# Performance work log

Hardware: AMD Instinct MI355X
Metric: run time of the kernel (lower is better)

The kernel has to match this reference:

```python
import jax, jax.numpy as jnp
import numpy as np

K, N, D, NCONV, E = 3, 30000, 128, 6, 480000


def _graph_conv(x, src, dst, ew, Wp, bp, Wrel, Wroot):
    # SAGE-style project=True: pre-project+relu source features
    h = jax.nn.relu(x @ Wp + bp)                    # [N, D]
    msg = ew[:, None] * h[src]                      # [E, D] gather
    agg = jax.ops.segment_sum(msg, dst, num_segments=N)
    cnt = jax.ops.segment_sum(jnp.ones_like(ew), dst, num_segments=N)
    agg = agg / jnp.maximum(cnt, 1.0)[:, None]      # mean aggregation
    return agg @ Wrel + x @ Wroot                   # GraphConv: lin_rel(agg)+lin_root(x), bias=False


def setup_inputs() -> dict:
    key = jax.random.key(0)
    ks = jax.random.split(key, 16)
    w = lambda k, s: (jax.random.normal(k, s, jnp.float32) * 0.05)
    inp = {
        "H_K_prev": jax.random.normal(ks[0], (K, N, D), jnp.float32),
        "edgelists": jax.random.randint(ks[1], (K, 2, E), 0, N, jnp.int32),
        "spec_weight": jax.random.uniform(ks[2], (K, NCONV, E), jnp.float32),
        # 6 stacked GraphConv params
        "Wp": w(ks[3], (NCONV, D, D)),
        "bp": jnp.zeros((NCONV, D), jnp.float32),
        "Wrel": w(ks[4], (NCONV, D, D)),
        "Wroot": w(ks[5], (NCONV, D, D)),
        # combine projection (7D -> 3D) and proj_linear (4D -> D)
        "W_comb": w(ks[6], ((NCONV + 1) * D, 3 * D)),
        "b_comb": jnp.zeros((3 * D,), jnp.float32),
        "W_pl": w(ks[7], (4 * D, D)),
        "b_pl": jnp.zeros((D,), jnp.float32),
        # LSTM (torch gate order i,f,g,o)
        "Wih": w(ks[8], (4 * D, D)),
        "Whh": w(ks[9], (4 * D, D)),
        "bih": jnp.zeros((4 * D,), jnp.float32),
        "bhh": jnp.zeros((4 * D,), jnp.float32),
    }
    return inp


def reference(H_K_prev, edgelists, spec_weight, Wp, bp, Wrel, Wroot,
              W_comb, b_comb, W_pl, b_pl, Wih, Whh, bih, bhh):
    outs = []
    for k in range(K):  # fixed small history loop
        Hk = H_K_prev[k]
        src, dst = edgelists[k, 0], edgelists[k, 1]
        feats = [Hk] + [
            _graph_conv(Hk, src, dst, spec_weight[k, i],
                        Wp[i], bp[i], Wrel[i], Wroot[i])
            for i in range(NCONV)
        ]
        cat = jnp.concatenate(feats, axis=1)               # [N, 7D]
        proj = jax.nn.relu(cat @ W_comb + b_comb)          # [N, 3D] (dropout=eval identity)
        outs.append(jnp.concatenate([Hk, proj], axis=1) @ W_pl + b_pl)  # [N, D]
    xs = jnp.stack(outs, 0)                                # [K, N, D] time-major

    def cell(carry, x_t):
        h, c = carry
        gates = x_t @ Wih.T + h @ Whh.T + bih + bhh        # [N, 4D]
        i, f, g, o = jnp.split(gates, 4, axis=1)
        c = jax.nn.sigmoid(f) * c + jax.nn.sigmoid(i) * jnp.tanh(g)
        h = jax.nn.sigmoid(o) * jnp.tanh(c)
        return (h, c), None

    z = jnp.zeros((N, D), xs.dtype)
    (h, _), _ = jax.lax.scan(cell, (z, z), xs)
    return jax.nn.relu(h)[None]                            # [1, N, D]
```

## Files before the change

kernel.cpp:

```cpp
#include <hip/hip_runtime.h>
#include <math.h>

constexpr int NN  = 30000;
constexpr int DIM = 128;
constexpr int KH  = 3;
constexpr int NC  = 6;
constexpr int EE  = 480000;
constexpr int NBLK = (NN + 255) / 256;

typedef __attribute__((ext_vector_type(8))) short short8;
typedef __attribute__((ext_vector_type(4))) float f32x4;
typedef __attribute__((ext_vector_type(2))) float f32x2;

__device__ __forceinline__ unsigned short f2bf(float f) {
    union { float f; unsigned int i; } c; c.f = f;
    unsigned int u = c.i;
    return (unsigned short)((u + 0x7fffu + ((u >> 16) & 1u)) >> 16);
}
__device__ __forceinline__ float bf2f(unsigned int u) {
    union { unsigned int i; float f; } c; c.i = u << 16; return c.f;
}
__device__ __forceinline__ unsigned int packbf(float x, float y) {
    return (unsigned int)f2bf(x) | ((unsigned int)f2bf(y) << 16);
}
__device__ __forceinline__ float fsig(float x) {
    return __builtin_amdgcn_rcpf(1.f + __expf(-x));
}
__device__ __forceinline__ float ftanh(float x) {
    return 2.f * fsig(2.f * x) - 1.f;
}

template<int OUT, bool RELU>
__global__ __launch_bounds__(256) void mgemm(
    const unsigned short* __restrict__ A1, int lda1,
    const unsigned short* __restrict__ A2, int lda2, int ksplit,
    const unsigned short* __restrict__ Bt, int ldb,
    const float* __restrict__ bias,
    void* __restrict__ Cv, int ldc,
    int M, int K, int nx)
{
    __shared__ __align__(16) unsigned char smem[2 * 128 * 80];
    unsigned char* As = smem;
    unsigned char* Bs = smem + 128 * 80;

    const int nwg  = gridDim.x;
    const int orig = blockIdx.x;
    const int q = nwg >> 3, r = nwg & 7;
    const int xcd = orig & 7, idx = orig >> 3;
    const int lin = (xcd < r ? xcd * (q + 1) : r * (q + 1) + (xcd - r) * q) + idx;
    const int bx = lin % nx, by = lin / nx;

    const int tid  = threadIdx.x;
    const int lane = tid & 63;
    const int w    = tid >> 6;
    const int wm   = w >> 1, wn = w & 1;
    const int lm   = lane & 15, lg = lane >> 4;
    const int bm   = by * 128;
    const int bn   = bx * 128;

    const int srow  = tid >> 1;
    const int shalf = tid & 1;

    f32x4 acc[4][4] = {};

    int arow = bm + srow; if (arow > M - 1) arow = M - 1;
    const int brow = bn + srow;

    for (int k0 = 0; k0 < K; k0 += 32) {
        const unsigned short* Ap; int la; int kk;
        if (k0 < ksplit) { Ap = A1; la = lda1; kk = k0; }
        else             { Ap = A2; la = lda2; kk = k0 - ksplit; }
        const float4* ga = (const float4*)(Ap + (size_t)arow * la + kk + shalf * 16);
        float4 a0 = ga[0], a1 = ga[1];
        const float4* gb = (const float4*)(Bt + (size_t)brow * ldb + k0 + shalf * 16);
        float4 b0 = gb[0], b1 = gb[1];

        __syncthreads();
        *(float4*)(As + srow * 80 + shalf * 32)      = a0;
        *(float4*)(As + srow * 80 + shalf * 32 + 16) = a1;
        *(float4*)(Bs + srow * 80 + shalf * 32)      = b0;
        *(float4*)(Bs + srow * 80 + shalf * 32 + 16) = b1;
        __syncthreads();

        short8 av[4], bv[4];
        #pragma unroll
        for (int f = 0; f < 4; ++f) {
            av[f] = *(const short8*)(As + (wm * 64 + f * 16 + lm) * 80 + lg * 16);
            bv[f] = *(const short8*)(Bs + (wn * 64 + f * 16 + lm) * 80 + lg * 16);
        }
        #pragma unroll
        for (int i = 0; i < 4; ++i)
            #pragma unroll
            for (int j = 0; j < 4; ++j)
                acc[i][j] = __builtin_amdgcn_mfma_f32_16x16x32_bf16(
                    av[i], bv[j], acc[i][j], 0, 0, 0);
    }

    #pragma unroll
    for (int i = 0; i < 4; ++i) {
        int row0 = bm + wm * 64 + i * 16 + lg * 4;
        #pragma unroll
        for (int j = 0; j < 4; ++j) {
            int col = bn + wn * 64 + j * 16 + lm;
            float bb = bias[col];
            #pragma unroll
            for (int r = 0; r < 4; ++r) {
                int row = row0 + r;
                if (row < M) {
                    float v = acc[i][j][r] + bb;
                    if (RELU) v = fmaxf(v, 0.f);
                    if (OUT == 0) {
                        ((unsigned short*)Cv)[(size_t)row * ldc + col] = f2bf(v);
                    } else {
                        unsigned int pk = __builtin_amdgcn_cvt_pk_fp8_f32(v, v, 0, false);
                        ((unsigned char*)Cv)[(size_t)row * ldc + col] = (unsigned char)pk;
                    }
                }
            }
        }
    }
}

__global__ void hist_kernel(const int* __restrict__ dst, int* __restrict__ cnt, int e)
{
    int i = blockIdx.x * 256 + threadIdx.x;
    if (i < e) atomicAdd(&cnt[dst[i]], 1);
}

__global__ __launch_bounds__(256) void scan_part(const int* __restrict__ cnt,
                                                 int* __restrict__ off,
                                                 int* __restrict__ bsum, int n)
{
    int lane = threadIdx.x & 63, wid = threadIdx.x >> 6;
    int i = blockIdx.x * 256 + threadIdx.x;
    int v = (i < n) ? cnt[i] : 0;
    int x = v;
    #pragma unroll
    for (int ofs = 1; ofs < 64; ofs <<= 1) {
        int t = __shfl_up(x, ofs, 64);
        if (lane >= ofs) x += t;
    }
    __shared__ int ws[4];
    if (lane == 63) ws[wid] = x;
    __syncthreads();
    int wo = 0;
    for (int j = 0; j < wid; ++j) wo += ws[j];
    if (i < n) off[i] = wo + x - v;
    if (threadIdx.x == 255) bsum[blockIdx.x] = wo + x;
}

__global__ __launch_bounds__(128) void scan_tops(const int* __restrict__ bsum,
                                                 int* __restrict__ btop, int nb)
{
    __shared__ int buf[128];
    int v = (threadIdx.x < nb) ? bsum[threadIdx.x] : 0;
    buf[threadIdx.x] = v;
    __syncthreads();
    #pragma unroll
    for (int ofs = 1; ofs < 128; ofs <<= 1) {
        int t = (threadIdx.x >= ofs) ? buf[threadIdx.x - ofs] : 0;
        __syncthreads();
        buf[threadIdx.x] += t;
        __syncthreads();
    }
    if (threadIdx.x < nb) btop[threadIdx.x] = buf[threadIdx.x] - v;
}

__global__ __launch_bounds__(256) void scan_add(int* __restrict__ off,
                                                const int* __restrict__ btop,
                                                int* __restrict__ cursor,
                                                int* __restrict__ cnt, int n)
{
    int i = blockIdx.x * 256 + threadIdx.x;
    if (i < n) {
        int o = off[i] + btop[blockIdx.x];
        off[i] = o;
        cursor[i] = o;
        cnt[i] = 0;
    }
    if (blockIdx.x == 0 && threadIdx.x == 0) off[n] = EE;
}

__global__ void fill_kernel(const int* __restrict__ src, const int* __restrict__ dst,
                            const float* __restrict__ sw,
                            int* __restrict__ cursor, int* __restrict__ csr_src,
                            uint2* __restrict__ swp, int e)
{
    int i = blockIdx.x * 256 + threadIdx.x;
    if (i >= e) return;
    int pos = atomicAdd(&cursor[dst[i]], 1);
    csr_src[pos] = src[i];
    uint2 lo, hi;
    lo.x = packbf(sw[i],                   sw[(size_t)EE + i]);
    lo.y = packbf(sw[2 * (size_t)EE + i],  0.f);
    hi.x = packbf(sw[3 * (size_t)EE + i],  sw[4 * (size_t)EE + i]);
    hi.y = packbf(sw[5 * (size_t)EE + i],  0.f);
    swp[(size_t)pos * 2]     = lo;
    swp[(size_t)pos * 2 + 1] = hi;
}

__global__ __launch_bounds__(256) void gather6(
    const unsigned char* __restrict__ h8,
    const uint2* __restrict__ swp,
    const int* __restrict__ csr_src,
    const int* __restrict__ off,
    unsigned short* __restrict__ agg)
{
    int wid  = threadIdx.x >> 6;
    int lane = threadIdx.x & 63;
    int node = blockIdx.x * 2 + (wid >> 1);
    int half = wid & 1;
    if (node >= NN) return;
    int s0 = off[node], s1 = off[node + 1];
    float a0 = 0.f, a1 = 0.f, b0 = 0.f, b1 = 0.f, c0 = 0.f, c1 = 0.f;
    const size_t hofs = (size_t)half * 384 + (size_t)lane * 2;

    int e = s0;
    for (; e + 3 < s1; e += 4) {
        int sA = csr_src[e],     sB = csr_src[e + 1];
        int sC = csr_src[e + 2], sD = csr_src[e + 3];
        uint2 wA = swp[(size_t)(e    ) * 2 + half];
        uint2 wB = swp[(size_t)(e + 1) * 2 + half];
        uint2 wC = swp[(size_t)(e + 2) * 2 + half];
        uint2 wD = swp[(size_t)(e + 3) * 2 + half];
        const unsigned short* rA = (const unsigned short*)(h8 + (size_t)sA * 768 + hofs);
        const unsigned short* rB = (const unsigned short*)(h8 + (size_t)sB * 768 + hofs);
        const unsigned short* rC = (const unsigned short*)(h8 + (size_t)sC * 768 + hofs);
        const unsigned short* rD = (const unsigned short*)(h8 + (size_t)sD * 768 + hofs);
        unsigned int pA0 = rA[0], pA1 = rA[64], pA2 = rA[128];
        unsigned int pB0 = rB[0], pB1 = rB[64], pB2 = rB[128];
        unsigned int pC0 = rC[0], pC1 = rC[64], pC2 = rC[128];
        unsigned int pD0 = rD[0], pD1 = rD[64], pD2 = rD[128];

        {
            float w0 = bf2f(wA.x & 0xffffu), w1 = bf2f(wA.x >> 16), w2 = bf2f(wA.y & 0xffffu);
            f32x2 h0 = __builtin_amdgcn_cvt_pk_f32_fp8(pA0, false);
            f32x2 h1 = __builtin_amdgcn_cvt_pk_f32_fp8(pA1, false);
            f32x2 h2 = __builtin_amdgcn_cvt_pk_f32_fp8(pA2, false);
            a0 += w0 * h0.x; a1 += w0 * h0.y;
            b0 += w1 * h1.x; b1 += w1 * h1.y;
            c0 += w2 * h2.x; c1 += w2 * h2.y;
        }
        {
            float w0 = bf2f(wB.x & 0xffffu), w1 = bf2f(wB.x >> 16), w2 = bf2f(wB.y & 0xffffu);
            f32x2 h0 = __builtin_amdgcn_cvt_pk_f32_fp8(pB0, false);
            f32x2 h1 = __builtin_amdgcn_cvt_pk_f32_fp8(pB1, false);
            f32x2 h2 = __builtin_amdgcn_cvt_pk_f32_fp8(pB2, false);
            a0 += w0 * h0.x; a1 += w0 * h0.y;
            b0 += w1 * h1.x; b1 += w1 * h1.y;
            c0 += w2 * h2.x; c1 += w2 * h2.y;
        }
        {
            float w0 = bf2f(wC.x & 0xffffu), w1 = bf2f(wC.x >> 16), w2 = bf2f(wC.y & 0xffffu);
            f32x2 h0 = __builtin_amdgcn_cvt_pk_f32_fp8(pC0, false);
            f32x2 h1 = __builtin_amdgcn_cvt_pk_f32_fp8(pC1, false);
            f32x2 h2 = __builtin_amdgcn_cvt_pk_f32_fp8(pC2, false);
            a0 += w0 * h0.x; a1 += w0 * h0.y;
            b0 += w1 * h1.x; b1 += w1 * h1.y;
            c0 += w2 * h2.x; c1 += w2 * h2.y;
        }
        {
            float w0 = bf2f(wD.x & 0xffffu), w1 = bf2f(wD.x >> 16), w2 = bf2f(wD.y & 0xffffu);
            f32x2 h0 = __builtin_amdgcn_cvt_pk_f32_fp8(pD0, false);
            f32x2 h1 = __builtin_amdgcn_cvt_pk_f32_fp8(pD1, false);
            f32x2 h2 = __builtin_amdgcn_cvt_pk_f32_fp8(pD2, false);
            a0 += w0 * h0.x; a1 += w0 * h0.y;
            b0 += w1 * h1.x; b1 += w1 * h1.y;
            c0 += w2 * h2.x; c1 += w2 * h2.y;
        }
    }
    for (; e < s1; ++e) {
        int src = csr_src[e];
        uint2 wv = swp[(size_t)e * 2 + half];
        float w0 = bf2f(wv.x & 0xffffu);
        float w1 = bf2f(wv.x >> 16);
        float w2 = bf2f(wv.y & 0xffffu);
        const unsigned short* hrow = (const unsigned short*)(h8 + (size_t)src * 768 + hofs);
        unsigned int p0 = hrow[0];
        unsigned int p1 = hrow[64];
        unsigned int p2 = hrow[128];
        f32x2 h0 = __builtin_amdgcn_cvt_pk_f32_fp8(p0, false);
        f32x2 h1 = __builtin_amdgcn_cvt_pk_f32_fp8(p1, false);
        f32x2 h2 = __builtin_amdgcn_cvt_pk_f32_fp8(p2, false);
        a0 += w0 * h0.x; a1 += w0 * h0.y;
        b0 += w1 * h1.x; b1 += w1 * h1.y;
        c0 += w2 * h2.x; c1 += w2 * h2.y;
    }
    float inv = 1.f / fmaxf((float)(s1 - s0), 1.f);
    unsigned int* orow = (unsigned int*)(agg + (size_t)node * 768) + 192 * half + lane;
    orow[0]   = packbf(a0 * inv, a1 * inv);
    orow[64]  = packbf(b0 * inv, b1 * inv);
    orow[128] = packbf(c0 * inv, c1 * inv);
}

__global__ void cvt_h(const float* __restrict__ Hk, unsigned int* __restrict__ out,
                      int total)
{
    int idx = blockIdx.x * 256 + threadIdx.x;
    if (idx >= total) return;
    float2 v = ((const float2*)Hk)[idx];
    out[idx] = packbf(v.x, v.y);
}

#define SWA32(r, b) ((r) * 512 + ((b) ^ (((r) & 7) << 4)))

__global__ __launch_bounds__(512) void lstm_fused(
    const unsigned short* __restrict__ xs,
    const unsigned short* __restrict__ Wt,
    const float* __restrict__ bsum,
    float* __restrict__ outp)
{
    __shared__ __align__(16) unsigned char AL[32 * 512];

    const int tid  = threadIdx.x;
    const int lane = tid & 63;
    const int w    = tid >> 6;
    const int lm   = lane & 15, lg = lane >> 4;
    const int node0 = blockIdx.x * 32;

    float bias[4];
    #pragma unroll
    for (int g = 0; g < 4; ++g)
        bias[g] = bsum[w * 64 + g * 16 + lm];

    short8 bw[8][4];
    #pragma unroll
    for (int ks = 0; ks < 8; ++ks)
        #pragma unroll
        for (int g = 0; g < 4; ++g)
            bw[ks][g] = *(const short8*)(Wt +
                (size_t)(w * 64 + g * 16 + lm) * 256 + ks * 32 + lg * 8);

    float cst[2][4] = {};

    float4 z4 = make_float4(0.f, 0.f, 0.f, 0.f);
    {
        int r = tid >> 4, gi = tid & 15;
        *(float4*)(AL + SWA32(r, 256 + gi * 16)) = z4;
    }

    for (int t = 0; t < KH; ++t) {
        const unsigned short* xsrc = xs + (size_t)t * NN * 128;
        {
            int r = tid >> 4, gi = tid & 15;
            int gr = node0 + r; if (gr >= NN) gr = NN - 1;
            float4 v = *(const float4*)(xsrc + (size_t)gr * 128 + gi * 8);
            *(float4*)(AL + SWA32(r, gi * 16)) = v;
        }
        __syncthreads();

        f32x4 acc[2][4] = {};
        #pragma unroll
        for (int ks = 0; ks < 8; ++ks) {
            short8 av[2];
            #pragma unroll
            for (int i = 0; i < 2; ++i)
                av[i] = *(const short8*)(AL + SWA32(i * 16 + lm, ks * 64 + lg * 16));
            #pragma unroll
            for (int g = 0; g < 4; ++g)
                #pragma unroll
                for (int i = 0; i < 2; ++i)
                    acc[i][g] = __builtin_amdgcn_mfma_f32_16x16x32_bf16(
                        av[i], bw[ks][g], acc[i][g], 0, 0, 0);
        }
        __syncthreads();

        #pragma unroll
        for (int i = 0; i < 2; ++i)
            #pragma unroll
            for (int r = 0; r < 4; ++r) {
                float giv = acc[i][0][r] + bias[0];
                float gfv = acc[i][1][r] + bias[1];
                float ggv = acc[i][2][r] + bias[2];
                float gov = acc[i][3][r] + bias[3];
                float si = fsig(giv);
                float sf = fsig(gfv);
                float so = fsig(gov);
                float cv = sf * cst[i][r] + si * ftanh(ggv);
                cst[i][r] = cv;
                float hv = so * ftanh(cv);
                int row = i * 16 + lg * 4 + r;
                int d   = w * 16 + lm;
                if (t < KH - 1) {
                    *(unsigned short*)(AL + SWA32(row, 256 + 2 * d)) = f2bf(hv);
                } else if (node0 + row < NN) {
                    outp[(size_t)(node0 + row) * 128 + d] = fmaxf(hv, 0.f);
                }
            }
    }
}

__global__ void wt_wp(const float* __restrict__ Wp, unsigned short* __restrict__ Wp_t)
{
    int idx = blockIdx.x * 256 + threadIdx.x;
    if (idx >= NC * DIM * DIM) return;
    int k = idx & 127, n = idx >> 7;
    int i = n >> 7, cc = n & 127;
    Wp_t[idx] = f2bf(Wp[(size_t)i * DIM * DIM + (size_t)k * DIM + cc]);
}

__global__ void wt_full(const float* __restrict__ Wcomb, const float* __restrict__ Wroot,
                        const float* __restrict__ Wrel, unsigned short* __restrict__ Wfull_t)
{
    int idx = blockIdx.x * 256 + threadIdx.x;
    if (idx >= 384 * 896) return;
    int m = idx % 896, n = idx / 896;
    float v;
    if (m < 128) {
        v = Wcomb[(size_t)m * 384 + n];
        for (int i = 0; i < NC; ++i) {
            const float* wr = Wroot + (size_t)i * DIM * DIM + (size_t)m * DIM;
            const float* wc = Wcomb + (size_t)(i + 1) * DIM * 384 + n;
            float s = 0.f;
            for (int k = 0; k < DIM; ++k) s += wr[k] * wc[(size_t)k * 384];
            v += s;
        }
    } else {
        int i = (m >> 7) - 1, rr = m & 127;
        const float* wr = Wrel + (size_t)i * DIM * DIM + (size_t)rr * DIM;
        const float* wc = Wcomb + (size_t)(i + 1) * DIM * 384 + n;
        float s = 0.f;
        for (int k = 0; k < DIM; ++k) s += wr[k] * wc[(size_t)k * 384];
        v = s;
    }
    Wfull_t[idx] = f2bf(v);
}

__global__ void wt_pl(const float* __restrict__ Wpl, unsigned short* __restrict__ Wpl_t)
{
    int idx = blockIdx.x * 256 + threadIdx.x;
    if (idx >= 128 * 512) return;
    int k = idx & 511, n = idx >> 9;
    Wpl_t[idx] = f2bf(Wpl[(size_t)k * DIM + n]);
}

__global__ void wt_lstm(const float* __restrict__ Wih, const float* __restrict__ Whh,
                        const float* __restrict__ bih, const float* __restrict__ bhh,
                        unsigned short* __restrict__ Wt, float* __restrict__ bsum)
{
    int idx = blockIdx.x * 256 + threadIdx.x;
    if (idx < 512) {
        int w = idx >> 6, rem = idx & 63, g = rem >> 4, d16 = rem & 15;
        int n = g * 128 + w * 16 + d16;
        bsum[idx] = bih[n] + bhh[n];
    }
    if (idx >= 512 * 256) return;
    int k = idx & 255, np = idx >> 8;
    int w = np >> 6, rem = np & 63, g = rem >> 4, d16 = rem & 15;
    int n = g * 128 + w * 16 + d16;
    Wt[idx] = f2bf(k < 128 ? Wih[(size_t)n * DIM + k]
                           : Whh[(size_t)n * DIM + (k - 128)]);
}

extern "C" void kernel_launch(void* const* d_in, const int* in_sizes, int n_in,
                              void* d_out, int out_size, void* d_ws, size_t ws_size,
                              hipStream_t stream)
{
    const float* H     = (const float*)d_in[0];
    const int*   EL    = (const int*)  d_in[1];
    const float* SW    = (const float*)d_in[2];
    const float* Wp    = (const float*)d_in[3];
    const float* bp    = (const float*)d_in[4];
    const float* Wrel  = (const float*)d_in[5];
    const float* Wroot = (const float*)d_in[6];
    const float* Wcomb = (const float*)d_in[7];
    const float* bcomb = (const float*)d_in[8];
    const float* Wpl   = (const float*)d_in[9];
    const float* bpl   = (const float*)d_in[10];
    const float* Wih   = (const float*)d_in[11];
    const float* Whh   = (const float*)d_in[12];
    const float* bih   = (const float*)d_in[13];
    const float* bhh   = (const float*)d_in[14];

    char* wp = (char*)d_ws;
    auto alloc = [&](size_t b) {
        char* p = wp; wp += (b + 255) & ~(size_t)255; return p;
    };
    unsigned short* Hbf  = (unsigned short*)alloc((size_t)NN * 128 * 2);
    unsigned char*  h8   = (unsigned char*) alloc((size_t)NN * 768);
    unsigned short* agg  = (unsigned short*)alloc((size_t)NN * 768 * 2);
    unsigned short* proj = (unsigned short*)alloc((size_t)NN * 384 * 2);
    unsigned short* xs   = (unsigned short*)alloc((size_t)KH * NN * 128 * 2);
    int* cnt     = (int*)alloc((size_t)NN * 4);
    int* off     = (int*)alloc((size_t)(NN + 1) * 4);
    int* cursor  = (int*)alloc((size_t)NN * 4);
    int* bsum    = (int*)alloc((size_t)NBLK * 4);
    int* btop    = (int*)alloc((size_t)NBLK * 4);
    int* csr_src = (int*)alloc((size_t)EE * 4);
    uint2* swp   = (uint2*)alloc((size_t)EE * 16);
    unsigned short* Wp_t     = (unsigned short*)alloc((size_t)768 * 128 * 2);
    unsigned short* Wfull_t  = (unsigned short*)alloc((size_t)384 * 896 * 2);
    unsigned short* Wpl_t    = (unsigned short*)alloc((size_t)128 * 512 * 2);
    unsigned short* WihWhh_t = (unsigned short*)alloc((size_t)512 * 256 * 2);
    float* bias_lstm         = (float*)alloc(512 * 4);

    wt_wp  <<<(NC * DIM * DIM + 255) / 256, 256, 0, stream>>>(Wp, Wp_t);
    wt_full<<<(384 * 896 + 255) / 256,     256, 0, stream>>>(Wcomb, Wroot, Wrel, Wfull_t);
    wt_pl  <<<(128 * 512 + 255) / 256,     256, 0, stream>>>(Wpl, Wpl_t);
    wt_lstm<<<(512 * 256 + 255) / 256,     256, 0, stream>>>(Wih, Whh, bih, bhh,
                                                             WihWhh_t, bias_lstm);

    hipMemsetAsync(cnt, 0, (size_t)NN * 4, stream);

    const int MB = (NN + 127) / 128;

    for (int k = 0; k < KH; ++k) {
        const float* Hk   = H + (size_t)k * NN * DIM;
        const int*   srcp = EL + (size_t)k * 2 * EE;
        const int*   dstp = srcp + EE;

        hist_kernel<<<(EE + 255) / 256, 256, 0, stream>>>(dstp, cnt, EE);
        scan_part<<<NBLK, 256, 0, stream>>>(cnt, off, bsum, NN);
        scan_tops<<<1, 128, 0, stream>>>(bsum, btop, NBLK);
        scan_add<<<NBLK, 256, 0, stream>>>(off, btop, cursor, cnt, NN);
        fill_kernel<<<(EE + 255) / 256, 256, 0, stream>>>(
            srcp, dstp, SW + (size_t)k * NC * EE, cursor, csr_src, swp, EE);

        cvt_h<<<(NN * 64 + 255) / 256, 256, 0, stream>>>(Hk, (unsigned int*)Hbf, NN * 64);

        mgemm<1, true><<<6 * MB, 256, 0, stream>>>(
            Hbf, 128, (const unsigned short*)nullptr, 0, 128,
            Wp_t, 128, bp, h8, 768, NN, 128, 6);

        gather6<<<NN / 2, 256, 0, stream>>>(h8, swp, csr_src, off, agg);

        mgemm<0, true><<<3 * MB, 256, 0, stream>>>(
            Hbf, 128, agg, 768, 128,
            Wfull_t, 896, bcomb, proj, 384, NN, 896, 3);

        mgemm<0, false><<<1 * MB, 256, 0, stream>>>(
            Hbf, 128, proj, 384, 128,
            Wpl_t, 512, bpl, xs + (size_t)k * NN * 128, 128, NN, 512, 1);
    }

    lstm_fused<<<(NN + 31) / 32, 512, 0, stream>>>(xs, WihWhh_t, bias_lstm,
                                                   (float*)d_out);
}
```

Before: 787.6 us.

## Batch CSR build across history steps and tile the weight-folding kernel

Builds the destination-sorted CSR for all three history graphs in a single pass: one histogram, one scan over 3N counts and one fill, in place of per-step launches. Converts all of H to bf16 up front. Replaces the naive per-element weight-fold kernel (each output doing a 128-long dot product strided by 384) with a shared-memory tiled fp32 GEMM. Replaces the strided transpose-convert kernels with a tiled transpose. Together these cut launch count and the serial weight-prep cost, at the price of larger workspace buffers for the three CSRs.

```diff
diff --git a/kernel.cpp b/kernel.cpp
--- a/kernel.cpp
+++ b/kernel.cpp
@@ -6,7 +6,7 @@
 constexpr int KH  = 3;
 constexpr int NC  = 6;
 constexpr int EE  = 480000;
-constexpr int NBLK = (NN + 255) / 256;
+constexpr int NBLK3 = (3 * NN + 255) / 256;
 
 typedef __attribute__((ext_vector_type(8))) short short8;
 typedef __attribute__((ext_vector_type(4))) float f32x4;
@@ -121,10 +121,14 @@
     }
 }
 
-__global__ void hist_kernel(const int* __restrict__ dst, int* __restrict__ cnt, int e)
+__global__ void hist3(const int* __restrict__ EL, int* __restrict__ cnt)
 {
     int i = blockIdx.x * 256 + threadIdx.x;
-    if (i < e) atomicAdd(&cnt[dst[i]], 1);
+    if (i >= 3 * EE) return;
+    int g = i / EE;
+    int e = i - g * EE;
+    int dst = EL[(size_t)g * 2 * EE + EE + e];
+    atomicAdd(&cnt[g * NN + dst], 1);
 }
 
 __global__ __launch_bounds__(256) void scan_part(const int* __restrict__ cnt,
@@ -149,15 +153,15 @@
     if (threadIdx.x == 255) bsum[blockIdx.x] = wo + x;
 }
 
-__global__ __launch_bounds__(128) void scan_tops(const int* __restrict__ bsum,
+__global__ __launch_bounds__(512) void scan_tops(const int* __restrict__ bsum,
                                                  int* __restrict__ btop, int nb)
 {
-    __shared__ int buf[128];
+    __shared__ int buf[512];
     int v = (threadIdx.x < nb) ? bsum[threadIdx.x] : 0;
     buf[threadIdx.x] = v;
     __syncthreads();
     #pragma unroll
-    for (int ofs = 1; ofs < 128; ofs <<= 1) {
+    for (int ofs = 1; ofs < 512; ofs <<= 1) {
         int t = (threadIdx.x >= ofs) ? buf[threadIdx.x - ofs] : 0;
         __syncthreads();
         buf[threadIdx.x] += t;
@@ -169,32 +173,35 @@
 __global__ __launch_bounds__(256) void scan_add(int* __restrict__ off,
                                                 const int* __restrict__ btop,
                                                 int* __restrict__ cursor,
-                                                int* __restrict__ cnt, int n)
+                                                int n, int etot)
 {
     int i = blockIdx.x * 256 + threadIdx.x;
     if (i < n) {
         int o = off[i] + btop[blockIdx.x];
         off[i] = o;
         cursor[i] = o;
-        cnt[i] = 0;
-    }
-    if (blockIdx.x == 0 && threadIdx.x == 0) off[n] = EE;
-}
-
-__global__ void fill_kernel(const int* __restrict__ src, const int* __restrict__ dst,
-                            const float* __restrict__ sw,
-                            int* __restrict__ cursor, int* __restrict__ csr_src,
-                            uint2* __restrict__ swp, int e)
+    }
+    if (blockIdx.x == 0 && threadIdx.x == 0) off[n] = etot;
+}
+
+__global__ void fill3(const int* __restrict__ EL, const float* __restrict__ SW,
+                      int* __restrict__ cursor, int* __restrict__ csr_src,
+                      uint2* __restrict__ swp)
 {
     int i = blockIdx.x * 256 + threadIdx.x;
-    if (i >= e) return;
-    int pos = atomicAdd(&cursor[dst[i]], 1);
-    csr_src[pos] = src[i];
+    if (i >= 3 * EE) return;
+    int g = i / EE;
+    int e = i - g * EE;
+    const int* base = EL + (size_t)g * 2 * EE;
+    int src = base[e], dst = base[EE + e];
+    int pos = atomicAdd(&cursor[g * NN + dst], 1);
+    csr_src[pos] = src;
+    const float* sw = SW + (size_t)g * NC * EE;
     uint2 lo, hi;
-    lo.x = packbf(sw[i],                   sw[(size_t)EE + i]);
-    lo.y = packbf(sw[2 * (size_t)EE + i],  0.f);
-    hi.x = packbf(sw[3 * (size_t)EE + i],  sw[4 * (size_t)EE + i]);
-    hi.y = packbf(sw[5 * (size_t)EE + i],  0.f);
+    lo.x = packbf(sw[e],                   sw[(size_t)EE + e]);
+    lo.y = packbf(sw[2 * (size_t)EE + e],  0.f);
+    hi.x = packbf(sw[3 * (size_t)EE + e],  sw[4 * (size_t)EE + e]);
+    hi.y = packbf(sw[5 * (size_t)EE + e],  0.f);
     swp[(size_t)pos * 2]     = lo;
     swp[(size_t)pos * 2 + 1] = hi;
 }
@@ -390,48 +397,82 @@
     }
 }
 
-__global__ void wt_wp(const float* __restrict__ Wp, unsigned short* __restrict__ Wp_t)
-{
-    int idx = blockIdx.x * 256 + threadIdx.x;
-    if (idx >= NC * DIM * DIM) return;
-    int k = idx & 127, n = idx >> 7;
-    int i = n >> 7, cc = n & 127;
-    Wp_t[idx] = f2bf(Wp[(size_t)i * DIM * DIM + (size_t)k * DIM + cc]);
-}
-
-__global__ void wt_full(const float* __restrict__ Wcomb, const float* __restrict__ Wroot,
-                        const float* __restrict__ Wrel, unsigned short* __restrict__ Wfull_t)
-{
-    int idx = blockIdx.x * 256 + threadIdx.x;
-    if (idx >= 384 * 896) return;
-    int m = idx % 896, n = idx / 896;
-    float v;
-    if (m < 128) {
-        v = Wcomb[(size_t)m * 384 + n];
-        for (int i = 0; i < NC; ++i) {
-            const float* wr = Wroot + (size_t)i * DIM * DIM + (size_t)m * DIM;
-            const float* wc = Wcomb + (size_t)(i + 1) * DIM * 384 + n;
-            float s = 0.f;
-            for (int k = 0; k < DIM; ++k) s += wr[k] * wc[(size_t)k * 384];
-            v += s;
-        }
-    } else {
-        int i = (m >> 7) - 1, rr = m & 127;
-        const float* wr = Wrel + (size_t)i * DIM * DIM + (size_t)rr * DIM;
-        const float* wc = Wcomb + (size_t)(i + 1) * DIM * 384 + n;
-        float s = 0.f;
-        for (int k = 0; k < DIM; ++k) s += wr[k] * wc[(size_t)k * 384];
-        v = s;
-    }
-    Wfull_t[idx] = f2bf(v);
-}
-
-__global__ void wt_pl(const float* __restrict__ Wpl, unsigned short* __restrict__ Wpl_t)
-{
-    int idx = blockIdx.x * 256 + threadIdx.x;
-    if (idx >= 128 * 512) return;
-    int k = idx & 511, n = idx >> 9;
-    Wpl_t[idx] = f2bf(Wpl[(size_t)k * DIM + n]);
+__global__ __launch_bounds__(256) void wt_fold(
+    const float* __restrict__ Wcomb,
+    const float* __restrict__ Wroot,
+    const float* __restrict__ Wrel,
+    unsigned short* __restrict__ Wfull_t)
+{
+    __shared__ __align__(16) float As[16][68];
+    __shared__ __align__(16) float Bs[16][68];
+    const int tid = threadIdx.x;
+    const int tx = tid & 15, ty = tid >> 4;
+    const int bm = blockIdx.y * 64;
+    const int bn = blockIdx.x * 64;
+    const bool root = (bm < 128);
+    const int i0 = root ? 0 : (bm >> 7) - 1;
+    const int i1 = root ? NC : i0 + 1;
+    const int mloc = bm & 127;
+    const int a_m = tid >> 2, a_k = (tid & 3) * 4;
+    const int b_k = tid >> 4, b_n = (tid & 15) * 4;
+
+    float acc[4][4] = {};
+
+    for (int i = i0; i < i1; ++i) {
+        const float* A = (root ? Wroot : Wrel) + (size_t)i * 128 * 128;
+        const float* B = Wcomb + (size_t)(i + 1) * 128 * 384;
+        for (int k0 = 0; k0 < 128; k0 += 16) {
+            float4 va = *(const float4*)(A + (size_t)(mloc + a_m) * 128 + k0 + a_k);
+            float4 vb = *(const float4*)(B + (size_t)(k0 + b_k) * 384 + bn + b_n);
+            __syncthreads();
+            As[a_k + 0][a_m] = va.x; As[a_k + 1][a_m] = va.y;
+            As[a_k + 2][a_m] = va.z; As[a_k + 3][a_m] = va.w;
+            *(float4*)&Bs[b_k][b_n] = vb;
+            __syncthreads();
+            #pragma unroll
+            for (int kk = 0; kk < 16; ++kk) {
+                float4 av = *(const float4*)&As[kk][ty * 4];
+                float4 bv = *(const float4*)&Bs[kk][tx * 4];
+                float a[4] = {av.x, av.y, av.z, av.w};
+                float b[4] = {bv.x, bv.y, bv.z, bv.w};
+                #pragma unroll
+                for (int ii = 0; ii < 4; ++ii)
+                    #pragma unroll
+                    for (int j = 0; j < 4; ++j)
+                        acc[ii][j] += a[ii] * b[j];
+            }
+        }
+    }
+
+    #pragma unroll
+    for (int ii = 0; ii < 4; ++ii) {
+        int m = bm + ty * 4 + ii;
+        #pragma unroll
+        for (int j = 0; j < 4; ++j) {
+            int n = bn + tx * 4 + j;
+            float v = acc[ii][j];
+            if (root) v += Wcomb[(size_t)m * 384 + n];
+            Wfull_t[(size_t)n * 896 + m] = f2bf(v);
+        }
+    }
+}
+
+__global__ __launch_bounds__(256) void tr_cvt(
+    const float* __restrict__ src, unsigned short* __restrict__ dst,
+    int R, int C)
+{
+    __shared__ float s[32][33];
+    const float* sb = src + (size_t)blockIdx.z * R * C;
+    unsigned short* db = dst + (size_t)blockIdx.z * R * C;
+    int r0 = blockIdx.y * 32, c0 = blockIdx.x * 32;
+    int tx = threadIdx.x & 31, ty = threadIdx.x >> 5;
+    #pragma unroll
+    for (int q = 0; q < 4; ++q)
+        s[ty + q * 8][tx] = sb[(size_t)(r0 + ty + q * 8) * C + c0 + tx];
+    __syncthreads();
+    #pragma unroll
+    for (int q = 0; q < 4; ++q)
+        db[(size_t)(c0 + ty + q * 8) * R + r0 + tx] = f2bf(s[tx][ty + q * 8]);
 }
 
 __global__ void wt_lstm(const float* __restrict__ Wih, const float* __restrict__ Whh,
@@ -476,60 +517,57 @@
     auto alloc = [&](size_t b) {
         char* p = wp; wp += (b + 255) & ~(size_t)255; return p;
     };
-    unsigned short* Hbf  = (unsigned short*)alloc((size_t)NN * 128 * 2);
+    unsigned short* Hbf  = (unsigned short*)alloc((size_t)3 * NN * 128 * 2);
     unsigned char*  h8   = (unsigned char*) alloc((size_t)NN * 768);
     unsigned short* agg  = (unsigned short*)alloc((size_t)NN * 768 * 2);
     unsigned short* proj = (unsigned short*)alloc((size_t)NN * 384 * 2);
     unsigned short* xs   = (unsigned short*)alloc((size_t)KH * NN * 128 * 2);
-    int* cnt     = (int*)alloc((size_t)NN * 4);
-    int* off     = (int*)alloc((size_t)(NN + 1) * 4);
-    int* cursor  = (int*)alloc((size_t)NN * 4);
-    int* bsum    = (int*)alloc((size_t)NBLK * 4);
-    int* btop    = (int*)alloc((size_t)NBLK * 4);
-    int* csr_src = (int*)alloc((size_t)EE * 4);
-    uint2* swp   = (uint2*)alloc((size_t)EE * 16);
+    int* cnt     = (int*)alloc((size_t)3 * NN * 4);
+    int* off     = (int*)alloc((size_t)(3 * NN + 1) * 4);
+    int* cursor  = (int*)alloc((size_t)3 * NN * 4);
+    int* bsum    = (int*)alloc((size_t)NBLK3 * 4);
+    int* btop    = (int*)alloc((size_t)NBLK3 * 4);
+    int* csr_src = (int*)alloc((size_t)3 * EE * 4);
+    uint2* swp   = (uint2*)alloc((size_t)3 * EE * 16);
     unsigned short* Wp_t     = (unsigned short*)alloc((size_t)768 * 128 * 2);
     unsigned short* Wfull_t  = (unsigned short*)alloc((size_t)384 * 896 * 2);
     unsigned short* Wpl_t    = (unsigned short*)alloc((size_t)128 * 512 * 2);
     unsigned short* WihWhh_t = (unsigned short*)alloc((size_t)512 * 256 * 2);
     float* bias_lstm         = (float*)alloc(512 * 4);
 
-    wt_wp  <<<(NC * DIM * DIM + 255) / 256, 256, 0, stream>>>(Wp, Wp_t);
-    wt_full<<<(384 * 896 + 255) / 256,     256, 0, stream>>>(Wcomb, Wroot, Wrel, Wfull_t);
-    wt_pl  <<<(128 * 512 + 255) / 256,     256, 0, stream>>>(Wpl, Wpl_t);
-    wt_lstm<<<(512 * 256 + 255) / 256,     256, 0, stream>>>(Wih, Whh, bih, bhh,
-                                                             WihWhh_t, bias_lstm);
-
-    hipMemsetAsync(cnt, 0, (size_t)NN * 4, stream);
+    tr_cvt<<<dim3(4, 4, 6), 256, 0, stream>>>(Wp, Wp_t, 128, 128);
+    wt_fold<<<dim3(6, 14), 256, 0, stream>>>(Wcomb, Wroot, Wrel, Wfull_t);
+    tr_cvt<<<dim3(4, 16, 1), 256, 0, stream>>>(Wpl, Wpl_t, 512, 128);
+    wt_lstm<<<(512 * 256 + 255) / 256, 256, 0, stream>>>(Wih, Whh, bih, bhh,
+                                                         WihWhh_t, bias_lstm);
+
+    hipMemsetAsync(cnt, 0, (size_t)3 * NN * 4, stream);
+    hist3<<<(3 * EE + 255) / 256, 256, 0, stream>>>(EL, cnt);
+    scan_part<<<NBLK3, 256, 0, stream>>>(cnt, off, bsum, 3 * NN);
+    scan_tops<<<1, 512, 0, stream>>>(bsum, btop, NBLK3);
+    scan_add<<<NBLK3, 256, 0, stream>>>(off, btop, cursor, 3 * NN, 3 * EE);
+    fill3<<<(3 * EE + 255) / 256, 256, 0, stream>>>(EL, SW, cursor, csr_src, swp);
+
+    cvt_h<<<(3 * NN * 64 + 255) / 256, 256, 0, stream>>>(H, (unsigned int*)Hbf,
+                                                         3 * NN * 64);
 
     const int MB = (NN + 127) / 128;
 
     for (int k = 0; k < KH; ++k) {
-        const float* Hk   = H + (size_t)k * NN * DIM;
-        const int*   srcp = EL + (size_t)k * 2 * EE;
-        const int*   dstp = srcp + EE;
-
-        hist_kernel<<<(EE + 255) / 256, 256, 0, stream>>>(dstp, cnt, EE);
-        scan_part<<<NBLK, 256, 0, stream>>>(cnt, off, bsum, NN);
-        scan_tops<<<1, 128, 0, stream>>>(bsum, btop, NBLK);
-        scan_add<<<NBLK, 256, 0, stream>>>(off, btop, cursor, cnt, NN);
-        fill_kernel<<<(EE + 255) / 256, 256, 0, stream>>>(
-            srcp, dstp, SW + (size_t)k * NC * EE, cursor, csr_src, swp, EE);
-
-        cvt_h<<<(NN * 64 + 255) / 256, 256, 0, stream>>>(Hk, (unsigned int*)Hbf, NN * 64);
+        const unsigned short* Hbk = Hbf + (size_t)k * NN * 128;
 
         mgemm<1, true><<<6 * MB, 256, 0, stream>>>(
-            Hbf, 128, (const unsigned short*)nullptr, 0, 128,
+            Hbk, 128, (const unsigned short*)nullptr, 0, 128,
             Wp_t, 128, bp, h8, 768, NN, 128, 6);
 
-        gather6<<<NN / 2, 256, 0, stream>>>(h8, swp, csr_src, off, agg);
+        gather6<<<NN / 2, 256, 0, stream>>>(h8, swp, csr_src, off + k * NN, agg);
 
         mgemm<0, true><<<3 * MB, 256, 0, stream>>>(
-            Hbf, 128, agg, 768, 128,
+            Hbk, 128, agg, 768, 128,
             Wfull_t, 896, bcomb, proj, 384, NN, 896, 3);
 
         mgemm<0, false><<<1 * MB, 256, 0, stream>>>(
-            Hbf, 128, proj, 384, 128,
+            Hbk, 128, proj, 384, 128,
             Wpl_t, 512, bpl, xs + (size_t)k * NN * 128, 128, NN, 512, 1);
     }
 
```

After: 738.3 us. -6.3%, faster.
